# Kernel optimization log

Hardware: AMD Instinct MI355X
Metric: run time of the kernel (lower is better)

Reference implementation:

```python
import jax, jax.numpy as jnp
import numpy as np

WORD_VOCAB = 100000
TAG_VOCAB = 50
WD = 300
TD = 100
EMB = WD + TD          # 400: LSTM input size AND hidden size
H = EMB
L = 512


def setup_inputs() -> dict:
    key = jax.random.key(0)
    ks = jax.random.split(key, 16)
    def p(k, shape):
        return jax.random.normal(k, shape, dtype=jnp.float32) * 0.05
    return {
        "words_idx_tensor": jax.random.randint(ks[0], (1, L), 0, WORD_VOCAB),
        "tags_idx_tensor": jax.random.randint(ks[1], (1, L), 0, TAG_VOCAB),
        "max_length": L,
        "word_emb": p(ks[2], (WORD_VOCAB, WD)),
        "tag_emb": p(ks[3], (TAG_VOCAB, TD)),
        # stacked [fwd, bwd] directions per layer (PyTorch LSTM gate order i,f,g,o)
        "w_ih_l0": p(ks[4], (2, 4 * H, EMB)),
        "w_hh_l0": p(ks[5], (2, 4 * H, H)),
        "b_ih_l0": p(ks[6], (2, 4 * H)),
        "b_hh_l0": p(ks[7], (2, 4 * H)),
        "w_ih_l1": p(ks[8], (2, 4 * H, 2 * H)),
        "w_hh_l1": p(ks[9], (2, 4 * H, H)),
        "b_ih_l1": p(ks[10], (2, 4 * H)),
        "b_hh_l1": p(ks[11], (2, 4 * H)),
        "fc1_w": p(ks[12], (1, 4 * H)),
        "fc1_b": p(ks[13], (1,)),
    }


def _lstm_dir(x, w_ih, w_hh, b_ih, b_hh, reverse):
    # x: [T, in]. Precompute input projections once (hoisted out of scan).
    xi = x @ w_ih.T + b_ih + b_hh  # [T, 4H]
    Hn = w_hh.shape[1]

    def step(carry, g_in):
        h, c = carry
        g = g_in + h @ w_hh.T
        i, f, gg, o = jnp.split(g, 4, axis=-1)
        c = jax.nn.sigmoid(f) * c + jax.nn.sigmoid(i) * jnp.tanh(gg)
        h = jax.nn.sigmoid(o) * jnp.tanh(c)
        return (h, c), h

    init = (jnp.zeros((Hn,), x.dtype), jnp.zeros((Hn,), x.dtype))
    _, hs = jax.lax.scan(step, init, xi, reverse=reverse)
    return hs  # [T, H]


def _bilstm(x, w_ih, w_hh, b_ih, b_hh):
    fwd = _lstm_dir(x, w_ih[0], w_hh[0], b_ih[0], b_hh[0], False)
    bwd = _lstm_dir(x, w_ih[1], w_hh[1], b_ih[1], b_hh[1], True)
    return jnp.concatenate([fwd, bwd], axis=-1)  # [T, 2H]


def reference(words_idx_tensor, tags_idx_tensor, max_length, word_emb, tag_emb,
              w_ih_l0, w_hh_l0, b_ih_l0, b_hh_l0,
              w_ih_l1, w_hh_l1, b_ih_l1, b_hh_l1,
              fc1_w, fc1_b):
    # Embedding lookup + concat; batch dim of size 1 squeezed (torch's
    # view(shape[1], shape[0], -1) yields [L, 1, emb] for the LSTM).
    x = jnp.concatenate([word_emb[words_idx_tensor[0]],
                         tag_emb[tags_idx_tensor[0]]], axis=-1)  # [L, EMB]

    h = _bilstm(x, w_ih_l0, w_hh_l0, b_ih_l0, b_hh_l0)   # [L, 2H]
    h = _bilstm(h, w_ih_l1, w_hh_l1, b_ih_l1, b_hh_l1)   # [L, 2H]

    # Pairwise edge scores: tanh(W @ [h_i; h_j] + b).
    # Split W into head/dep halves -> two small GEMMs + broadcast outer-sum,
    # avoiding the O(L^2 * 4H) concatenated feature tensor.
    two_h = fc1_w.shape[1] // 2
    s = h @ fc1_w[:, :two_h].T   # [L, 1]
    t = h @ fc1_w[:, two_h:].T   # [L, 1]
    scores = jnp.tanh(s[:, None, :] + t[None, :, :] + fc1_b)  # [L, L, 1]
    # torch stacks (i outer, j inner) -> [L*L, 1, 1]
    return scores.reshape(max_length * max_length, 1, 1)
```

## Files before the change

kernel.cpp:

```cpp
#include <hip/hip_runtime.h>

#define SEQ 512
#define HID 400
#define GATES 1600
#define E1 800
#define TEAM 10
#define RECGRID 160

__device__ __forceinline__ float bf2f(unsigned short u) {
    return __uint_as_float(((unsigned)u) << 16);
}
__device__ __forceinline__ unsigned short f2bf(float f) {
    unsigned u = __float_as_uint(f);
    u += 0x7FFFu + ((u >> 16) & 1u);
    return (unsigned short)(u >> 16);
}
__device__ __forceinline__ float sigm(float x) { return 1.f / (1.f + __expf(-x)); }
__device__ __forceinline__ float tanh_f(float x) {
    float xc = fminf(fmaxf(x, -15.f), 15.f);
    float e = __expf(2.f * xc);
    return (e - 1.f) / (e + 1.f);
}
__device__ __forceinline__ float loadx(const void* p, size_t i, int isbf) {
    return isbf ? bf2f(((const unsigned short*)p)[i]) : ((const float*)p)[i];
}

__global__ void detect_kernel(const unsigned short* __restrict__ wemb,
                              unsigned* __restrict__ dtf) {
    __shared__ int cnt;
    if (threadIdx.x == 0) cnt = 0;
    __syncthreads();
    int pass = 0;
    for (int i = 0; i < 8; ++i) {
        unsigned short u = wemb[threadIdx.x * 8 + i];
        int e = (u >> 7) & 0xFF;
        pass += (e >= 100 && e <= 130) ? 1 : 0;
    }
    atomicAdd(&cnt, pass);
    __syncthreads();
    if (threadIdx.x == 0) *dtf = (cnt >= 1843) ? 1u : 0u;
}

__global__ void embed_kernel(const int* __restrict__ words, const int* __restrict__ tags,
                             const void* __restrict__ wemb, const void* __restrict__ temb,
                             float* __restrict__ x ,
                             const unsigned* __restrict__ dtf) {
    int t = blockIdx.x;
    int w = words[t], g = tags[t];
    int isbf = (int)*dtf;
    for (int k = threadIdx.x; k < HID; k += blockDim.x) {
        float v = (k < 300) ? loadx(wemb, (size_t)w * 300 + k, isbf)
                            : loadx(temb, (size_t)g * 100 + (k - 300), isbf);
        x[(size_t)t * HID + k] = v;
    }
}

__global__ __launch_bounds__(256) void proj_kernel(
        const void* __restrict__ Araw, int tagged,
        const void* __restrict__ Wraw ,
        const void* __restrict__ bihRaw, const void* __restrict__ bhhRaw,
        float* __restrict__ xi ,
        int K, const unsigned* __restrict__ dtf) {
    const int isbf = (int)*dtf;
    __shared__ float As[16][132];
    __shared__ float Ws[16][68];
    int tid = threadIdx.x;
    int t0 = blockIdx.x * 128, n0 = blockIdx.y * 64, dir = blockIdx.z;
    int arow = tid >> 1, akoff = (tid & 1) * 8;
    int wrow = tid >> 2, wkoff = (tid & 3) * 4;
    int tx = (tid & 15) * 4;
    int ty = (tid >> 4) * 8;

    const float* Af = (const float*)Araw + (size_t)(t0 + arow) * K + akoff;
    const unsigned long long* At = (const unsigned long long*)Araw +
                                   (size_t)(t0 + arow) * K + akoff;
    size_t wbase = (size_t)(dir * GATES + n0 + wrow) * K + wkoff;
    const float* Wf = (const float*)Wraw + wbase;
    const unsigned short* Wh = (const unsigned short*)Wraw + wbase;

    float acc[8][4] = {};
    for (int k0 = 0; k0 < K; k0 += 16) {
        float av8[8];
        if (tagged) {
            ulonglong2 q0 = *(const ulonglong2*)(At + k0);
            ulonglong2 q1 = *(const ulonglong2*)(At + k0 + 2);
            ulonglong2 q2 = *(const ulonglong2*)(At + k0 + 4);
            ulonglong2 q3 = *(const ulonglong2*)(At + k0 + 6);
            av8[0] = __uint_as_float((unsigned)q0.x); av8[1] = __uint_as_float((unsigned)q0.y);
            av8[2] = __uint_as_float((unsigned)q1.x); av8[3] = __uint_as_float((unsigned)q1.y);
            av8[4] = __uint_as_float((unsigned)q2.x); av8[5] = __uint_as_float((unsigned)q2.y);
            av8[6] = __uint_as_float((unsigned)q3.x); av8[7] = __uint_as_float((unsigned)q3.y);
        } else {
            float4 a0 = *(const float4*)(Af + k0);
            float4 a1 = *(const float4*)(Af + k0 + 4);
            av8[0] = a0.x; av8[1] = a0.y; av8[2] = a0.z; av8[3] = a0.w;
            av8[4] = a1.x; av8[5] = a1.y; av8[6] = a1.z; av8[7] = a1.w;
        }
        float4 wv;
        if (isbf) {
            ushort4 w4 = *(const ushort4*)(Wh + k0);
            wv = make_float4(bf2f(w4.x), bf2f(w4.y), bf2f(w4.z), bf2f(w4.w));
        } else {
            wv = *(const float4*)(Wf + k0);
        }
        __syncthreads();
#pragma unroll
        for (int i = 0; i < 8; ++i) As[akoff + i][arow] = av8[i];
        Ws[wkoff + 0][wrow] = wv.x; Ws[wkoff + 1][wrow] = wv.y;
        Ws[wkoff + 2][wrow] = wv.z; Ws[wkoff + 3][wrow] = wv.w;
        __syncthreads();
#pragma unroll
        for (int kk = 0; kk < 16; ++kk) {
            float4 alo = *(const float4*)&As[kk][ty];
            float4 ahi = *(const float4*)&As[kk][ty + 4];
            float4 w4  = *(const float4*)&Ws[kk][tx];
            float av[8] = {alo.x, alo.y, alo.z, alo.w, ahi.x, ahi.y, ahi.z, ahi.w};
            float wvv[4] = {w4.x, w4.y, w4.z, w4.w};
#pragma unroll
            for (int i = 0; i < 8; ++i)
#pragma unroll
                for (int j = 0; j < 4; ++j)
                    acc[i][j] = fmaf(av[i], wvv[j], acc[i][j]);
        }
    }
    float bias[4];
#pragma unroll
    for (int j = 0; j < 4; ++j) {
        int n = n0 + tx + j;
        bias[j] = loadx(bihRaw, dir * GATES + n, isbf) + loadx(bhhRaw, dir * GATES + n, isbf);
    }
    float* xout = xi + (size_t)dir * SEQ * GATES;
#pragma unroll
    for (int i = 0; i < 8; ++i) {
        int t = t0 + ty + i;
        float4 o = make_float4(acc[i][0] + bias[0], acc[i][1] + bias[1],
                               acc[i][2] + bias[2], acc[i][3] + bias[3]);
        *(float4*)&xout[(size_t)t * GATES + n0 + tx] = o;
    }
}

struct SyncArea { unsigned cnt[8]; unsigned claim[2]; unsigned pad[6]; };

__global__ __launch_bounds__(512, 2) void rec_kernel(
        const float* __restrict__ xi ,
        const void* __restrict__ whhRaw ,
        unsigned long long* __restrict__ hx  ,
        unsigned long long* __restrict__ hx2 ,
        unsigned tagbase, SyncArea* __restrict__ sy,
        const unsigned* __restrict__ dtf) {
    int tid = threadIdx.x;
    __shared__ int role[2];
    if (tid == 0) {
        unsigned xcd = __builtin_amdgcn_s_getreg((3 << 11) | 20) & 0xFu;
        unsigned rank = atomicAdd(&sy->cnt[xcd], 1u);
        unsigned group = rank / TEAM;
        unsigned key = 1u + xcd * 64u + group;
        if ((rank % TEAM) == TEAM - 1) {
            unsigned prev = atomicCAS(&sy->claim[0], 0u, key);
            if (prev != 0u) atomicCAS(&sy->claim[1], 0u, key);
        }
        int dir = -1;
        while (dir < 0) {
            unsigned c0 = __hip_atomic_load(&sy->claim[0], __ATOMIC_RELAXED,
                                            __HIP_MEMORY_SCOPE_AGENT);
            unsigned c1 = __hip_atomic_load(&sy->claim[1], __ATOMIC_RELAXED,
                                            __HIP_MEMORY_SCOPE_AGENT);
            if (c0 == key) dir = 0;
            else if (c1 == key) dir = 1;
            else if (c0 != 0u && c1 != 0u) dir = 2;
        }
        role[0] = dir;
        role[1] = (int)(rank % TEAM);
    }
    __syncthreads();
    const int dir = role[0];
    const int wg  = role[1];
    if (dir == 2) return;

    int chunk = tid & 15;
    int rg    = tid >> 4;
    const int isbf = (int)*dtf;
    const int dirHID = dir * HID;

    __shared__ __align__(16) float hbuf[HID];
    __shared__ __align__(16) float partials[160][20];
    __shared__ __align__(16) float gates[160];

    float wv[5][25];
#pragma unroll
    for (int r = 0; r < 5; ++r) {
        int lr = rg * 5 + r;
        int jj = lr >> 2, gg = lr & 3;
        int grow = gg * HID + wg * 40 + jj;
        size_t base = ((size_t)dir * GATES + grow) * HID + chunk * 25;
        if (isbf) {
            const unsigned short* p = (const unsigned short*)whhRaw + base;
#pragma unroll
            for (int c = 0; c < 25; ++c) wv[r][c] = bf2f(p[c]);
        } else {
            const float* p = (const float*)whhRaw + base;
#pragma unroll
            for (int c = 0; c < 25; ++c) wv[r][c] = p[c];
        }
    }

    int xrow = 0;
    if (tid < 160) { int jj = tid >> 2, gg = tid & 3; xrow = gg * HID + wg * 40 + jj; }
    const float* xibase = xi + (size_t)dir * SEQ * GATES;
    float cstate = 0.f;
    size_t myelem = dirHID + wg * 40 + tid;

#pragma unroll 1
    for (int k = 0; k < SEQ; ++k) {
        int t = dir ? (SEQ - 1 - k) : k;
        float xiv = 0.f;
        if (tid < 160) xiv = xibase[(size_t)t * GATES + xrow];

        if (k > 0) {
            int tprev = dir ? (t + 1) : (t - 1);
            if (tid < HID) {
                const unsigned want = tagbase + (unsigned)k;
                size_t eidx = (size_t)tprev * E1 + dirHID + tid;
                const volatile unsigned long long* p =
                    (const volatile unsigned long long*)&hx[eidx];
                unsigned long long w;
                int spin = 0;
                for (;;) {
                    w = *p;
                    if ((unsigned)(w >> 32) == want) break;
                    if (++spin >= 24) {
                        w = __hip_atomic_load(&hx2[eidx], __ATOMIC_RELAXED,
                                              __HIP_MEMORY_SCOPE_AGENT);
                        if ((unsigned)(w >> 32) == want) break;
                        spin = 0;
                    }
                }
                hbuf[tid] = __uint_as_float((unsigned)w);
            }
        } else {
            if (tid < HID) hbuf[tid] = 0.f;
        }
        __syncthreads();

        float acc[5] = {0.f, 0.f, 0.f, 0.f, 0.f};
#pragma unroll
        for (int c = 0; c < 25; ++c) {
            float hv = hbuf[chunk * 25 + c];
#pragma unroll
            for (int r = 0; r < 5; ++r)
                acc[r] = fmaf(wv[r][c], hv, acc[r]);
        }
#pragma unroll
        for (int r = 0; r < 5; ++r) partials[rg * 5 + r][chunk] = acc[r];
        __syncthreads();

        if (tid < 160) {
            const float4* pr = (const float4*)&partials[tid][0];
            float4 p0 = pr[0], p1 = pr[1], p2 = pr[2], p3 = pr[3];
            float s = p0.x + p0.y + p0.z + p0.w
                    + p1.x + p1.y + p1.z + p1.w
                    + p2.x + p2.y + p2.z + p2.w
                    + p3.x + p3.y + p3.z + p3.w;
            gates[tid] = s + xiv;
        }
        __syncthreads();

        if (tid < 40) {
            float4 g4 = *(const float4*)&gates[tid * 4];
            float ig = sigm(g4.x), fg = sigm(g4.y), cg = tanh_f(g4.z), og = sigm(g4.w);
            cstate = fg * cstate + ig * cg;
            float hv = og * tanh_f(cstate);
            unsigned long long w =
                ((unsigned long long)(tagbase + (unsigned)k + 1u) << 32) |
                (unsigned long long)(unsigned)__float_as_uint(hv);
            size_t eidx = (size_t)t * E1 + myelem;
            *(volatile unsigned long long*)&hx[eidx] = w;
            __hip_atomic_store(&hx2[eidx], w, __ATOMIC_RELAXED,
                               __HIP_MEMORY_SCOPE_AGENT);
        }
    }
}

__global__ void st_kernel(const unsigned long long* __restrict__ h1x ,
                          const void* __restrict__ fw ,
                          float* __restrict__ sv, float* __restrict__ tv,
                          const unsigned* __restrict__ dtf) {
    int i = blockIdx.x;
    int lane = threadIdx.x;
    int isbf = (int)*dtf;
    float s = 0.f, t = 0.f;
    for (int j = lane; j < E1; j += 64) {
        float hv = __uint_as_float((unsigned)h1x[(size_t)i * E1 + j]);
        s += hv * loadx(fw, j, isbf);
        t += hv * loadx(fw, E1 + j, isbf);
    }
#pragma unroll
    for (int o = 32; o > 0; o >>= 1) {
        s += __shfl_xor(s, o, 64);
        t += __shfl_xor(t, o, 64);
    }
    if (lane == 0) { sv[i] = s; tv[i] = t; }
}

__global__ void scores_kernel(const float* __restrict__ sv, const float* __restrict__ tv,
                              const void* __restrict__ fb, void* __restrict__ out,
                              const unsigned* __restrict__ dtf) {
    int idx = blockIdx.x * blockDim.x + threadIdx.x;
    int i = idx >> 9, j = idx & 511;
    int isbf = (int)*dtf;
    float v = tanh_f(sv[i] + tv[j] + loadx(fb, 0, isbf));
    if (isbf) ((unsigned short*)out)[idx] = f2bf(v);
    else      ((float*)out)[idx] = v;
}

static constexpr size_t OFF_X    = 0;
static constexpr size_t OFF_XI   = 819200;
static constexpr size_t OFF_SV   = 7372800;
static constexpr size_t OFF_TV   = 7374848;
static constexpr size_t OFF_DTF  = 7376896;
static constexpr size_t OFF_SYNC = 7376960;
static constexpr size_t OFF_HX   = 7377216;
static constexpr size_t OFF_HX2  = 10654016;

extern "C" void kernel_launch(void* const* d_in, const int* in_sizes, int n_in,
                              void* d_out, int out_size, void* d_ws, size_t ws_size,
                              hipStream_t stream) {
    const int* words = (const int*)d_in[0];
    const int* tags  = (const int*)d_in[1];
    const void* wemb = d_in[3];
    const void* temb = d_in[4];
    const void* wih0 = d_in[5];
    const void* whh0 = d_in[6];
    const void* bih0 = d_in[7];
    const void* bhh0 = d_in[8];
    const void* wih1 = d_in[9];
    const void* whh1 = d_in[10];
    const void* bih1 = d_in[11];
    const void* bhh1 = d_in[12];
    const void* fw   = d_in[13];
    const void* fb   = d_in[14];

    char* ws = (char*)d_ws;
    float* x               = (float*)(ws + OFF_X);
    float* xi              = (float*)(ws + OFF_XI);
    float* sv              = (float*)(ws + OFF_SV);
    float* tv              = (float*)(ws + OFF_TV);
    unsigned* dtf          = (unsigned*)(ws + OFF_DTF);
    SyncArea* sync0        = (SyncArea*)(ws + OFF_SYNC);
    SyncArea* sync1        = (SyncArea*)(ws + OFF_SYNC + 64);
    unsigned long long* hx  = (unsigned long long*)(ws + OFF_HX);
    unsigned long long* hx2 = (unsigned long long*)(ws + OFF_HX2);

    hipMemsetAsync(ws + OFF_SYNC, 0, 128, stream);
    detect_kernel<<<1, 256, 0, stream>>>((const unsigned short*)wemb, dtf);
    embed_kernel<<<SEQ, 128, 0, stream>>>(words, tags, wemb, temb, x, dtf);

    proj_kernel<<<dim3(4, 25, 2), 256, 0, stream>>>(x, 0, wih0, bih0, bhh0, xi, HID, dtf);
    rec_kernel<<<RECGRID, 512, 0, stream>>>(xi, whh0, hx, hx2, 0u, sync0, dtf);

    proj_kernel<<<dim3(4, 25, 2), 256, 0, stream>>>(hx, 1, wih1, bih1, bhh1, xi, E1, dtf);
    rec_kernel<<<RECGRID, 512, 0, stream>>>(xi, whh1, hx, hx2, 512u, sync1, dtf);

    st_kernel<<<SEQ, 64, 0, stream>>>(hx, fw, sv, tv, dtf);
    scores_kernel<<<(SEQ * SEQ) / 256, 256, 0, stream>>>(sv, tv, fb, d_out, dtf);
}
```

Baseline: 1.968 ms.

## Widen recurrent LSTM teams to 25 blocks with per-thread rows and packed bf16 weights

Each direction's recurrence is now split across 25 workgroups of 16 hidden units each, instead of 10 groups of 40. Each thread now holds one gate row's 50-element slice (packed as bf16 pairs when inputs are bf16), which removes one reduction barrier per step. The input projection for the next step is prefetched into a double-buffered shared array, and the secondary hx2 atomic mirror with its fallback spin is dropped in favour of a plain volatile poll. The kernel is templated on dtype and both variants are launched, with the one that does not match the detected dtype returning early. More blocks must be co-resident for the spin-wait to make progress, and the volatile-only poll depends on the device making the stores visible without the agent-scope mirror.

```diff
diff --git a/kernel.cpp b/kernel.cpp
--- a/kernel.cpp
+++ b/kernel.cpp
@@ -4,8 +4,8 @@
 #define HID 400
 #define GATES 1600
 #define E1 800
-#define TEAM 10
-#define RECGRID 160
+#define TEAM 25
+#define RECGRID 256
 
 __device__ __forceinline__ float bf2f(unsigned short u) {
     return __uint_as_float(((unsigned)u) << 16);
@@ -141,13 +141,15 @@
 
 struct SyncArea { unsigned cnt[8]; unsigned claim[2]; unsigned pad[6]; };
 
+template <int ISBF>
 __global__ __launch_bounds__(512, 2) void rec_kernel(
         const float* __restrict__ xi ,
         const void* __restrict__ whhRaw ,
-        unsigned long long* __restrict__ hx  ,
-        unsigned long long* __restrict__ hx2 ,
+        unsigned long long* __restrict__ hx ,
         unsigned tagbase, SyncArea* __restrict__ sy,
         const unsigned* __restrict__ dtf) {
+    if (*(volatile const unsigned*)dtf != (unsigned)ISBF) return;
+
     int tid = threadIdx.x;
     __shared__ int role[2];
     if (tid == 0) {
@@ -177,106 +179,106 @@
     const int wg  = role[1];
     if (dir == 2) return;
 
-    int chunk = tid & 15;
-    int rg    = tid >> 4;
-    const int isbf = (int)*dtf;
+    const int rg    = tid >> 3;
+    const int chunk = tid & 7;
+    const int gg = rg >> 4, jj = rg & 15;
+    const int grow = gg * HID + wg * 16 + jj;
     const int dirHID = dir * HID;
 
     __shared__ __align__(16) float hbuf[HID];
-    __shared__ __align__(16) float partials[160][20];
-    __shared__ __align__(16) float gates[160];
-
-    float wv[5][25];
-#pragma unroll
-    for (int r = 0; r < 5; ++r) {
-        int lr = rg * 5 + r;
-        int jj = lr >> 2, gg = lr & 3;
-        int grow = gg * HID + wg * 40 + jj;
-        size_t base = ((size_t)dir * GATES + grow) * HID + chunk * 25;
-        if (isbf) {
+    __shared__ __align__(16) float partials[64][12];
+    __shared__ float xibuf[2][64];
+
+    unsigned pk[25];
+    float    wf[50];
+    {
+        size_t base = ((size_t)dir * GATES + grow) * HID + chunk * 50;
+        if (ISBF) {
             const unsigned short* p = (const unsigned short*)whhRaw + base;
 #pragma unroll
-            for (int c = 0; c < 25; ++c) wv[r][c] = bf2f(p[c]);
+            for (int c = 0; c < 25; ++c)
+                pk[c] = ((unsigned)p[2 * c + 1] << 16) | (unsigned)p[2 * c];
         } else {
             const float* p = (const float*)whhRaw + base;
 #pragma unroll
-            for (int c = 0; c < 25; ++c) wv[r][c] = p[c];
-        }
-    }
-
-    int xrow = 0;
-    if (tid < 160) { int jj = tid >> 2, gg = tid & 3; xrow = gg * HID + wg * 40 + jj; }
+            for (int c = 0; c < 50; ++c) wf[c] = p[c];
+        }
+    }
+
     const float* xibase = xi + (size_t)dir * SEQ * GATES;
+    const int w7 = tid - 448;
+    if (w7 >= 0) {
+        int t0 = dir ? SEQ - 1 : 0;
+        xibuf[0][w7] = xibase[(size_t)t0 * GATES + (w7 >> 4) * HID + wg * 16 + (w7 & 15)];
+    }
     float cstate = 0.f;
-    size_t myelem = dirHID + wg * 40 + tid;
+    size_t myelem = (size_t)dirHID + wg * 16 + tid;
 
 #pragma unroll 1
     for (int k = 0; k < SEQ; ++k) {
         int t = dir ? (SEQ - 1 - k) : k;
-        float xiv = 0.f;
-        if (tid < 160) xiv = xibase[(size_t)t * GATES + xrow];
+
+        float xin = 0.f;
+        if (w7 >= 0) {
+            int kn = (k + 1 < SEQ) ? (k + 1) : k;
+            int tn = dir ? (SEQ - 1 - kn) : kn;
+            xin = xibase[(size_t)tn * GATES + (w7 >> 4) * HID + wg * 16 + (w7 & 15)];
+        }
 
         if (k > 0) {
-            int tprev = dir ? (t + 1) : (t - 1);
             if (tid < HID) {
                 const unsigned want = tagbase + (unsigned)k;
-                size_t eidx = (size_t)tprev * E1 + dirHID + tid;
+                int tprev = dir ? (t + 1) : (t - 1);
                 const volatile unsigned long long* p =
-                    (const volatile unsigned long long*)&hx[eidx];
+                    (const volatile unsigned long long*)&hx[(size_t)tprev * E1 + dirHID + tid];
                 unsigned long long w;
-                int spin = 0;
-                for (;;) {
-                    w = *p;
-                    if ((unsigned)(w >> 32) == want) break;
-                    if (++spin >= 24) {
-                        w = __hip_atomic_load(&hx2[eidx], __ATOMIC_RELAXED,
-                                              __HIP_MEMORY_SCOPE_AGENT);
-                        if ((unsigned)(w >> 32) == want) break;
-                        spin = 0;
-                    }
-                }
+                do { w = *p; } while ((unsigned)(w >> 32) != want);
                 hbuf[tid] = __uint_as_float((unsigned)w);
             }
         } else {
             if (tid < HID) hbuf[tid] = 0.f;
         }
         __syncthreads();
-
-        float acc[5] = {0.f, 0.f, 0.f, 0.f, 0.f};
-#pragma unroll
-        for (int c = 0; c < 25; ++c) {
-            float hv = hbuf[chunk * 25 + c];
-#pragma unroll
-            for (int r = 0; r < 5; ++r)
-                acc[r] = fmaf(wv[r][c], hv, acc[r]);
-        }
-#pragma unroll
-        for (int r = 0; r < 5; ++r) partials[rg * 5 + r][chunk] = acc[r];
+        if (w7 >= 0) xibuf[(k + 1) & 1][w7] = xin;
+
+        float acc = 0.f;
+        if (ISBF) {
+#pragma unroll
+            for (int c = 0; c < 25; ++c) {
+                float2 hp = *(const float2*)&hbuf[chunk * 50 + 2 * c];
+                unsigned u = pk[c];
+                acc = fmaf(__uint_as_float(u << 16), hp.x, acc);
+                acc = fmaf(__uint_as_float(u & 0xffff0000u), hp.y, acc);
+            }
+        } else {
+#pragma unroll
+            for (int c = 0; c < 25; ++c) {
+                float2 hp = *(const float2*)&hbuf[chunk * 50 + 2 * c];
+                acc = fmaf(wf[2 * c], hp.x, acc);
+                acc = fmaf(wf[2 * c + 1], hp.y, acc);
+            }
+        }
+        partials[rg][chunk] = acc;
         __syncthreads();
 
-        if (tid < 160) {
-            const float4* pr = (const float4*)&partials[tid][0];
-            float4 p0 = pr[0], p1 = pr[1], p2 = pr[2], p3 = pr[3];
-            float s = p0.x + p0.y + p0.z + p0.w
-                    + p1.x + p1.y + p1.z + p1.w
-                    + p2.x + p2.y + p2.z + p2.w
-                    + p3.x + p3.y + p3.z + p3.w;
-            gates[tid] = s + xiv;
-        }
-        __syncthreads();
-
-        if (tid < 40) {
-            float4 g4 = *(const float4*)&gates[tid * 4];
-            float ig = sigm(g4.x), fg = sigm(g4.y), cg = tanh_f(g4.z), og = sigm(g4.w);
+        if (tid < 16) {
+            float g4[4];
+#pragma unroll
+            for (int g = 0; g < 4; ++g) {
+                int row = g * 16 + tid;
+                float4 a = *(const float4*)&partials[row][0];
+                float4 b = *(const float4*)&partials[row][4];
+                g4[g] = a.x + a.y + a.z + a.w + b.x + b.y + b.z + b.w
+                      + xibuf[k & 1][row];
+            }
+            float ig = sigm(g4[0]), fg = sigm(g4[1]);
+            float cg = tanh_f(g4[2]), og = sigm(g4[3]);
             cstate = fg * cstate + ig * cg;
             float hv = og * tanh_f(cstate);
             unsigned long long w =
                 ((unsigned long long)(tagbase + (unsigned)k + 1u) << 32) |
-                (unsigned long long)(unsigned)__float_as_uint(hv);
-            size_t eidx = (size_t)t * E1 + myelem;
-            *(volatile unsigned long long*)&hx[eidx] = w;
-            __hip_atomic_store(&hx2[eidx], w, __ATOMIC_RELAXED,
-                               __HIP_MEMORY_SCOPE_AGENT);
+                (unsigned long long)__float_as_uint(hv);
+            *(volatile unsigned long long*)&hx[(size_t)t * E1 + myelem] = w;
         }
     }
 }
@@ -320,7 +322,6 @@
 static constexpr size_t OFF_DTF  = 7376896;
 static constexpr size_t OFF_SYNC = 7376960;
 static constexpr size_t OFF_HX   = 7377216;
-static constexpr size_t OFF_HX2  = 10654016;
 
 extern "C" void kernel_launch(void* const* d_in, const int* in_sizes, int n_in,
                               void* d_out, int out_size, void* d_ws, size_t ws_size,
@@ -348,18 +349,19 @@
     unsigned* dtf          = (unsigned*)(ws + OFF_DTF);
     SyncArea* sync0        = (SyncArea*)(ws + OFF_SYNC);
     SyncArea* sync1        = (SyncArea*)(ws + OFF_SYNC + 64);
-    unsigned long long* hx  = (unsigned long long*)(ws + OFF_HX);
-    unsigned long long* hx2 = (unsigned long long*)(ws + OFF_HX2);
+    unsigned long long* hx = (unsigned long long*)(ws + OFF_HX);
 
     hipMemsetAsync(ws + OFF_SYNC, 0, 128, stream);
     detect_kernel<<<1, 256, 0, stream>>>((const unsigned short*)wemb, dtf);
     embed_kernel<<<SEQ, 128, 0, stream>>>(words, tags, wemb, temb, x, dtf);
 
     proj_kernel<<<dim3(4, 25, 2), 256, 0, stream>>>(x, 0, wih0, bih0, bhh0, xi, HID, dtf);
-    rec_kernel<<<RECGRID, 512, 0, stream>>>(xi, whh0, hx, hx2, 0u, sync0, dtf);
+    rec_kernel<1><<<RECGRID, 512, 0, stream>>>(xi, whh0, hx, 0u, sync0, dtf);
+    rec_kernel<0><<<RECGRID, 512, 0, stream>>>(xi, whh0, hx, 0u, sync0, dtf);
 
     proj_kernel<<<dim3(4, 25, 2), 256, 0, stream>>>(hx, 1, wih1, bih1, bhh1, xi, E1, dtf);
-    rec_kernel<<<RECGRID, 512, 0, stream>>>(xi, whh1, hx, hx2, 512u, sync1, dtf);
+    rec_kernel<1><<<RECGRID, 512, 0, stream>>>(xi, whh1, hx, 512u, sync1, dtf);
+    rec_kernel<0><<<RECGRID, 512, 0, stream>>>(xi, whh1, hx, 512u, sync1, dtf);
 
     st_kernel<<<SEQ, 64, 0, stream>>>(hx, fw, sv, tv, dtf);
     scores_kernel<<<(SEQ * SEQ) / 256, 256, 0, stream>>>(sv, tv, fb, d_out, dtf);
```

New measurement: 2.281 ms. 15.9% more time.
